# Kernel tuning notes

Hardware: AMD Instinct MI355X
Metric: run time of the kernel (lower is better)

The kernel has to match this reference:

```python
import jax, jax.numpy as jnp
import numpy as np

D_MODEL = 512
PRED_LEN = 720
CHANNELS = 321
BATCH = 64

def setup_inputs() -> dict:
    key = jax.random.key(0)
    k_x, k_w, k_b = jax.random.split(key, 3)
    x = jax.random.normal(k_x, (BATCH, CHANNELS, D_MODEL), dtype=jnp.float32)
    # Per-channel Linear(d_model -> pred_len): stacked weights/biases.
    # (Original inits to zero; random here for a meaningful numeric baseline.)
    W = jax.random.normal(k_w, (CHANNELS, D_MODEL, PRED_LEN), dtype=jnp.float32) * (1.0 / np.sqrt(D_MODEL))
    b = jax.random.normal(k_b, (CHANNELS, PRED_LEN), dtype=jnp.float32) * 0.01
    return {"x": x, "W": W, "b": b}

def reference(x, W, b):
    # Fused form of the per-channel loop: out[:, c] = x[:, c] @ W_c + b_c
    # x: [B, C, D], W: [C, D, P], b: [C, P] -> out: [B, C, P]
    return jnp.einsum('bcd,cdp->bcp', x, W) + b[None, :, :]
```

## Files before the change

kernel.cpp:

```cpp
#include <hip/hip_runtime.h>

#define NB 64
#define NC 321
#define ND 512
#define NP 720

#define BN 128
#define BK 64
#define NPT 6

typedef __bf16 bf16x8 __attribute__((ext_vector_type(8)));
typedef float f32x4 __attribute__((ext_vector_type(4)));
typedef unsigned short u16x8 __attribute__((ext_vector_type(8)));
typedef unsigned short u16x4 __attribute__((ext_vector_type(4)));

__device__ __forceinline__ unsigned short f2bf(float f) {
    unsigned int u = __builtin_bit_cast(unsigned int, f);
    return (unsigned short)((u + 0x7FFFu + ((u >> 16) & 1u)) >> 16);
}

__global__ __launch_bounds__(256) void GenLayer_57191784514055_kernel(
    const float* __restrict__ x, const float* __restrict__ W,
    const float* __restrict__ bias, float* __restrict__ out)
{
    const int pt = blockIdx.x;
    const int c  = blockIdx.y;
    const int p0 = pt * BN;

    const int tid  = threadIdx.x;
    const int lane = tid & 63;
    const int wid  = tid >> 6;
    const int lr   = lane & 15;
    const int qd   = lane >> 4;

    __shared__ __align__(16) unsigned short lds[(64 + BN) * BK];

    int a_lidx[4];
    const float* a_gp[4];
#pragma unroll
    for (int i = 0; i < 4; ++i) {
        int task = tid + i * 256;
        int m  = task >> 4;
        int kk = (task & 15) << 2;
        a_lidx[i] = m * BK + ((((kk >> 3) ^ (m & 7)) << 3) | (kk & 7));
        a_gp[i]   = x + (size_t)m * (NC * ND) + (size_t)c * ND + kk;
    }

    int b_pl[2], b_dl[2];
    const float* b_gp[2];
    bool b_ok[2];
#pragma unroll
    for (int i = 0; i < 2; ++i) {
        int T  = tid + i * 256;
        int pq = (T & 7) | (((T >> 6) & 1) << 3) | (((T >> 8) & 1) << 4);
        int dq = ((T >> 3) & 7) | (((T >> 7) & 1) << 3);
        b_pl[i] = pq << 2;
        b_dl[i] = dq << 2;
        int pg = p0 + b_pl[i];
        b_ok[i] = (pg < NP);
        b_gp[i] = W + (size_t)c * (ND * NP) + (size_t)b_dl[i] * NP + pg;
    }

    const int mbase = (wid & 1) << 5;
    const int nbase = (wid >> 1) << 6;

    f32x4 acc[2][4];
#pragma unroll
    for (int ms = 0; ms < 2; ++ms)
#pragma unroll
        for (int ns = 0; ns < 4; ++ns)
            acc[ms][ns] = (f32x4){0.f, 0.f, 0.f, 0.f};

    for (int kt = 0; kt < ND / BK; ++kt) {
        if (kt) __syncthreads();

        f32x4 av[4];
#pragma unroll
        for (int i = 0; i < 4; ++i)
            av[i] = *(const f32x4*)(a_gp[i] + kt * BK);

        f32x4 bv[2][4];
#pragma unroll
        for (int i = 0; i < 2; ++i) {
#pragma unroll
            for (int r = 0; r < 4; ++r) {
                if (b_ok[i])
                    bv[i][r] = *(const f32x4*)(b_gp[i] + (size_t)(kt * BK + r) * NP);
                else
                    bv[i][r] = (f32x4){0.f, 0.f, 0.f, 0.f};
            }
        }

#pragma unroll
        for (int i = 0; i < 4; ++i) {
            u16x4 v = { f2bf(av[i][0]), f2bf(av[i][1]), f2bf(av[i][2]), f2bf(av[i][3]) };
            *(u16x4*)(&lds[a_lidx[i]]) = v;
        }
#pragma unroll
        for (int i = 0; i < 2; ++i) {
#pragma unroll
            for (int j = 0; j < 4; ++j) {
                int p = b_pl[i] + j;
                int d = b_dl[i];
                u16x4 v = { f2bf(bv[i][0][j]), f2bf(bv[i][1][j]),
                            f2bf(bv[i][2][j]), f2bf(bv[i][3][j]) };
                int idx = 64 * BK + p * BK + ((((d >> 3) ^ (p & 7)) << 3) | (d & 7));
                *(u16x4*)(&lds[idx]) = v;
            }
        }

        __syncthreads();

#pragma unroll
        for (int ks = 0; ks < 2; ++ks) {
            const int gk = ks * 4 + qd;
            bf16x8 af[2], bfr[4];
#pragma unroll
            for (int ms = 0; ms < 2; ++ms) {
                int row = mbase + ms * 16 + lr;
                af[ms] = __builtin_bit_cast(bf16x8,
                    *(const u16x8*)(&lds[row * BK + ((gk ^ (row & 7)) << 3)]));
            }
#pragma unroll
            for (int ns = 0; ns < 4; ++ns) {
                int n = nbase + ns * 16 + lr;
                bfr[ns] = __builtin_bit_cast(bf16x8,
                    *(const u16x8*)(&lds[64 * BK + n * BK + ((gk ^ (n & 7)) << 3)]));
            }
#pragma unroll
            for (int ms = 0; ms < 2; ++ms)
#pragma unroll
                for (int ns = 0; ns < 4; ++ns)
                    acc[ms][ns] = __builtin_amdgcn_mfma_f32_16x16x32_bf16(
                        af[ms], bfr[ns], acc[ms][ns], 0, 0, 0);
        }
    }

#pragma unroll
    for (int ns = 0; ns < 4; ++ns) {
        int p = p0 + nbase + ns * 16 + lr;
        if (p < NP) {
            float bb = bias[c * NP + p];
#pragma unroll
            for (int ms = 0; ms < 2; ++ms) {
                int row0 = mbase + ms * 16 + qd * 4;
                float* op = out + (size_t)row0 * (NC * NP) + (size_t)c * NP + p;
#pragma unroll
                for (int r = 0; r < 4; ++r)
                    op[(size_t)r * (NC * NP)] = acc[ms][ns][r] + bb;
            }
        }
    }
}

extern "C" void kernel_launch(void* const* d_in, const int* in_sizes, int n_in,
                              void* d_out, int out_size, void* d_ws, size_t ws_size,
                              hipStream_t stream) {
    const float* x  = (const float*)d_in[0];
    const float* W  = (const float*)d_in[1];
    const float* b  = (const float*)d_in[2];
    float* out      = (float*)d_out;
    dim3 grid(NPT, NC);
    GenLayer_57191784514055_kernel<<<grid, dim3(256), 0, stream>>>(x, W, b, out);
}
```

Baseline: 665.6 us.

## Pre-convert x and W to bf16 in workspace and load tiles via global_load_lds

```diff
diff --git a/kernel.cpp b/kernel.cpp
--- a/kernel.cpp
+++ b/kernel.cpp
@@ -4,6 +4,7 @@
 #define NC 321
 #define ND 512
 #define NP 720
+#define NPPAD 768
 
 #define BN 128
 #define BK 64
@@ -12,15 +13,72 @@
 typedef __bf16 bf16x8 __attribute__((ext_vector_type(8)));
 typedef float f32x4 __attribute__((ext_vector_type(4)));
 typedef unsigned short u16x8 __attribute__((ext_vector_type(8)));
-typedef unsigned short u16x4 __attribute__((ext_vector_type(4)));
+
+typedef __attribute__((address_space(1))) const void* gas_ptr;
+typedef __attribute__((address_space(3))) void* las_ptr;
+#define GLLD16(gp, lp) __builtin_amdgcn_global_load_lds((gas_ptr)(gp), (las_ptr)(lp), 16, 0, 0)
 
 __device__ __forceinline__ unsigned short f2bf(float f) {
     unsigned int u = __builtin_bit_cast(unsigned int, f);
     return (unsigned short)((u + 0x7FFFu + ((u >> 16) & 1u)) >> 16);
 }
 
-__global__ __launch_bounds__(256) void GenLayer_57191784514055_kernel(
-    const float* __restrict__ x, const float* __restrict__ W,
+__global__ __launch_bounds__(256) void convert_x_kernel(
+    const float* __restrict__ x, unsigned short* __restrict__ xb)
+{
+    size_t base = ((size_t)blockIdx.x * 256 + threadIdx.x) * 8;
+    f32x4 a = *(const f32x4*)(x + base);
+    f32x4 b = *(const f32x4*)(x + base + 4);
+    u16x8 v = { f2bf(a[0]), f2bf(a[1]), f2bf(a[2]), f2bf(a[3]),
+                f2bf(b[0]), f2bf(b[1]), f2bf(b[2]), f2bf(b[3]) };
+    *(u16x8*)(xb + base) = v;
+}
+
+__global__ __launch_bounds__(256) void convert_W_kernel(
+    const float* __restrict__ W, unsigned short* __restrict__ Wt)
+{
+    const int p0 = blockIdx.x * 64;
+    const int d0 = blockIdx.y * 64;
+    const int c  = blockIdx.z;
+    const int t  = threadIdx.x;
+
+    __shared__ __align__(16) float tile[64 * 65];
+
+    const float* src = W + (size_t)c * (ND * NP);
+#pragma unroll
+    for (int i = 0; i < 4; ++i) {
+        int r   = (t >> 4) + i * 16;
+        int col = (t & 15) * 4;
+        int p   = p0 + col;
+        f32x4 v;
+        if (p + 3 < NP) {
+            v = *(const f32x4*)(src + (size_t)(d0 + r) * NP + p);
+        } else {
+#pragma unroll
+            for (int j = 0; j < 4; ++j)
+                v[j] = (p + j < NP) ? src[(size_t)(d0 + r) * NP + p + j] : 0.f;
+        }
+        *(f32x4*)(&tile[r * 65 + col]) = v;
+    }
+    __syncthreads();
+
+#pragma unroll
+    for (int i = 0; i < 2; ++i) {
+        int task = t + i * 256;
+        int pp = task >> 3;
+        int dg = task & 7;
+        if (p0 + pp < NP) {
+            u16x8 v;
+#pragma unroll
+            for (int j = 0; j < 8; ++j)
+                v[j] = f2bf(tile[(dg * 8 + j) * 65 + pp]);
+            *(u16x8*)(Wt + ((size_t)c * NPPAD + p0 + pp) * ND + d0 + dg * 8) = v;
+        }
+    }
+}
+
+__global__ __launch_bounds__(256) void gemm_kernel(
+    const unsigned short* __restrict__ xb, const unsigned short* __restrict__ Wt,
     const float* __restrict__ bias, float* __restrict__ out)
 {
     const int pt = blockIdx.x;
@@ -32,34 +90,28 @@
     const int wid  = tid >> 6;
     const int lr   = lane & 15;
     const int qd   = lane >> 4;
+    const int lrow = lane >> 3;
+    const int g    = lane & 7;
 
     __shared__ __align__(16) unsigned short lds[(64 + BN) * BK];
 
-    int a_lidx[4];
-    const float* a_gp[4];
+    const unsigned short* a_src[2];
+#pragma unroll
+    for (int i = 0; i < 2; ++i) {
+        int ca = wid * 2 + i;
+        int m  = ca * 8 + lrow;
+        a_src[i] = xb + (size_t)m * (NC * ND) + (size_t)c * ND + ((g ^ (m & 7)) << 3);
+    }
+    const unsigned short* b_src[4];
 #pragma unroll
     for (int i = 0; i < 4; ++i) {
-        int task = tid + i * 256;
-        int m  = task >> 4;
-        int kk = (task & 15) << 2;
-        a_lidx[i] = m * BK + ((((kk >> 3) ^ (m & 7)) << 3) | (kk & 7));
-        a_gp[i]   = x + (size_t)m * (NC * ND) + (size_t)c * ND + kk;
+        int cb = wid * 4 + i;
+        int n  = cb * 8 + lrow;
+        b_src[i] = Wt + ((size_t)c * NPPAD + p0 + n) * ND + ((g ^ (n & 7)) << 3);
     }
-
-    int b_pl[2], b_dl[2];
-    const float* b_gp[2];
-    bool b_ok[2];
-#pragma unroll
-    for (int i = 0; i < 2; ++i) {
-        int T  = tid + i * 256;
-        int pq = (T & 7) | (((T >> 6) & 1) << 3) | (((T >> 8) & 1) << 4);
-        int dq = ((T >> 3) & 7) | (((T >> 7) & 1) << 3);
-        b_pl[i] = pq << 2;
-        b_dl[i] = dq << 2;
-        int pg = p0 + b_pl[i];
-        b_ok[i] = (pg < NP);
-        b_gp[i] = W + (size_t)c * (ND * NP) + (size_t)b_dl[i] * NP + pg;
-    }
+    unsigned short* a_dst[2] = { &lds[(wid * 2 + 0) * 512], &lds[(wid * 2 + 1) * 512] };
+    unsigned short* b_dst[4] = { &lds[4096 + (wid * 4 + 0) * 512], &lds[4096 + (wid * 4 + 1) * 512],
+                                 &lds[4096 + (wid * 4 + 2) * 512], &lds[4096 + (wid * 4 + 3) * 512] };
 
     const int mbase = (wid & 1) << 5;
     const int nbase = (wid >> 1) << 6;
@@ -74,40 +126,14 @@
     for (int kt = 0; kt < ND / BK; ++kt) {
         if (kt) __syncthreads();
 
-        f32x4 av[4];
 #pragma unroll
-        for (int i = 0; i < 4; ++i)
-            av[i] = *(const f32x4*)(a_gp[i] + kt * BK);
-
-        f32x4 bv[2][4];
+        for (int i = 0; i < 2; ++i) GLLD16(a_src[i], a_dst[i]);
 #pragma unroll
-        for (int i = 0; i < 2; ++i) {
+        for (int i = 0; i < 4; ++i) GLLD16(b_src[i], b_dst[i]);
 #pragma unroll
-            for (int r = 0; r < 4; ++r) {
-                if (b_ok[i])
-                    bv[i][r] = *(const f32x4*)(b_gp[i] + (size_t)(kt * BK + r) * NP);
-                else
-                    bv[i][r] = (f32x4){0.f, 0.f, 0.f, 0.f};
-            }
-        }
-
+        for (int i = 0; i < 2; ++i) a_src[i] += BK;
 #pragma unroll
-        for (int i = 0; i < 4; ++i) {
-            u16x4 v = { f2bf(av[i][0]), f2bf(av[i][1]), f2bf(av[i][2]), f2bf(av[i][3]) };
-            *(u16x4*)(&lds[a_lidx[i]]) = v;
-        }
-#pragma unroll
-        for (int i = 0; i < 2; ++i) {
-#pragma unroll
-            for (int j = 0; j < 4; ++j) {
-                int p = b_pl[i] + j;
-                int d = b_dl[i];
-                u16x4 v = { f2bf(bv[i][0][j]), f2bf(bv[i][1][j]),
-                            f2bf(bv[i][2][j]), f2bf(bv[i][3][j]) };
-                int idx = 64 * BK + p * BK + ((((d >> 3) ^ (p & 7)) << 3) | (d & 7));
-                *(u16x4*)(&lds[idx]) = v;
-            }
-        }
+        for (int i = 0; i < 4; ++i) b_src[i] += BK;
 
         __syncthreads();
 
@@ -125,7 +151,7 @@
             for (int ns = 0; ns < 4; ++ns) {
                 int n = nbase + ns * 16 + lr;
                 bfr[ns] = __builtin_bit_cast(bf16x8,
-                    *(const u16x8*)(&lds[64 * BK + n * BK + ((gk ^ (n & 7)) << 3)]));
+                    *(const u16x8*)(&lds[4096 + n * BK + ((gk ^ (n & 7)) << 3)]));
             }
 #pragma unroll
             for (int ms = 0; ms < 2; ++ms)
@@ -160,6 +186,11 @@
     const float* W  = (const float*)d_in[1];
     const float* b  = (const float*)d_in[2];
     float* out      = (float*)d_out;
-    dim3 grid(NPT, NC);
-    GenLayer_57191784514055_kernel<<<grid, dim3(256), 0, stream>>>(x, W, b, out);
+
+    unsigned short* Wt = (unsigned short*)d_ws;
+    unsigned short* xb = (unsigned short*)((char*)d_ws + (size_t)NC * NPPAD * ND * 2);
+
+    convert_x_kernel<<<dim3(5136), dim3(256), 0, stream>>>(x, xb);
+    convert_W_kernel<<<dim3(12, 8, NC), dim3(256), 0, stream>>>(W, Wt);
+    gemm_kernel<<<dim3(NPT, NC), dim3(256), 0, stream>>>(xb, Wt, b, out);
 }
```

New measurement: 757.6 us. 1.14x slower.
